# Kernel optimization log

Hardware: AMD Instinct MI355X
Metric: run time of the kernel (lower is better)

The kernel has to match this reference:

```python
import jax, jax.numpy as jnp
import numpy as np

# ---- static config (mirrors CE defaults) ----
PS = 7        # patch size
WS = 27       # search window (per side)
S0 = 4        # query stride (stride0)
KS = 100      # k_s: top-k kept by search
KA = 100      # k_a: top-k used for aggregation
SCALE = 10.0  # softmax_scale
CI = 16       # inter_channels


def conv2d(x, w, b, pad):
    y = jax.lax.conv_general_dilated(
        x, w, (1, 1), [(pad, pad), (pad, pad)],
        dimension_numbers=("NCHW", "OIHW", "NCHW"))
    return y + b[None, :, None, None]


def all_patches(v):
    """[T,C,H,W] -> [T, H*W, C*PS*PS]; top-left anchored PSxPS patches,
    edge-clamped at the border (dnls-style bounded patch extraction)."""
    t, c, h, w = v.shape
    ii = jnp.clip(jnp.arange(h)[:, None] + jnp.arange(PS)[None, :], 0, h - 1)
    jj = jnp.clip(jnp.arange(w)[:, None] + jnp.arange(PS)[None, :], 0, w - 1)
    p = v[:, :, ii][:, :, :, :, jj]          # [T,C,H,PS,W,PS]
    p = p.transpose(0, 2, 4, 1, 3, 5)        # [T,H,W,C,PS,PS]
    return p.reshape(t, h * w, c * PS * PS)


def setup_inputs():
    key = jax.random.key(0)
    ks = jax.random.split(key, 4)
    vid = jax.random.normal(ks[0], (4, 64, 128, 128), jnp.float32)
    g_w = jax.random.normal(ks[1], (CI, 64, 3, 3), jnp.float32) * 0.05
    g_b = jnp.zeros((CI,), jnp.float32)
    theta_w = jax.random.normal(ks[2], (CI, 64, 1, 1), jnp.float32) * 0.1
    theta_b = jnp.zeros((CI,), jnp.float32)
    return {"vid": vid, "g_w": g_w, "g_b": g_b,
            "theta_w": theta_w, "theta_b": theta_b}


def reference(vid, g_w, g_b, theta_w, theta_b):
    t, c, h, w = vid.shape
    nH, nW = h // S0, w // S0
    Q, N = nH * nW, h * w

    # feature extraction (g -> search features, theta -> aggregation values)
    v1 = conv2d(vid, g_w, g_b, 1)          # [T,CI,H,W]
    v2 = conv2d(vid, theta_w, theta_b, 0)  # [T,CI,H,W]

    # windowed k-NN patch search: query grid (stride0) vs all keys (stride1=1)
    P1 = all_patches(v1)                                    # [T,N,D]
    qis = jnp.arange(nH) * S0
    qjs = jnp.arange(nW) * S0
    qflat = (qis[:, None] * w + qjs[None, :]).reshape(-1)   # [Q]
    Pq = P1[:, qflat]                                       # [T,Q,D]
    scores = jnp.einsum("tqd,tnd->tqn", Pq, P1)             # [T,Q,N]

    off = jnp.arange(WS) - WS // 2
    ci = jnp.clip(qis[:, None] + off, 0, h - 1)             # [nH,WS]
    cj = jnp.clip(qjs[:, None] + off, 0, w - 1)             # [nW,WS]
    cand = (ci[:, None, :, None] * w + cj[None, :, None, :]).reshape(Q, WS * WS)
    dists = jnp.take_along_axis(scores, cand[None], axis=2)  # [T,Q,WS*WS]

    d_k, widx = jax.lax.top_k(dists, KS)                    # [T,Q,KS]
    inds = jnp.take_along_axis(jnp.broadcast_to(cand[None], dists.shape),
                               widx, axis=2)                # flat key positions

    # top-k softmax aggregation weights
    wgt = jax.nn.softmax(d_k[..., :KA] * SCALE, axis=-1)    # [T,Q,KA]
    inds_a = inds[..., :KA]

    # wpsum: weighted sum of value patches gathered at neighbor indices,
    # expressed as sparse-scatter matrix @ dense patch matrix
    A = jnp.zeros((t, Q, N), scores.dtype).at[
        jnp.arange(t)[:, None, None],
        jnp.arange(Q)[None, :, None],
        inds_a].add(wgt)                                    # [T,Q,N]
    P2 = all_patches(v2)                                    # [T,N,D]
    z = jnp.einsum("tqn,tnd->tqd", A, P2)                   # [T,Q,CI*PS*PS]

    # ifold: scatter-add overlapping patches + count normalization
    z = z.reshape(t, Q, CI, PS, PS).transpose(0, 2, 1, 3, 4)
    z = z.reshape(t, CI, Q * PS * PS)
    ri = jnp.clip(qis[:, None] + jnp.arange(PS), 0, h - 1)  # [nH,PS]
    rj = jnp.clip(qjs[:, None] + jnp.arange(PS), 0, w - 1)  # [nW,PS]
    pix = (ri[:, None, :, None] * w + rj[None, :, None, :]).reshape(-1)
    Y = jnp.zeros((t, CI, N), z.dtype).at[:, :, pix].add(z)
    Zc = jnp.zeros((N,), z.dtype).at[pix].add(1.0)
    y = (Y / Zc).reshape(t, CI, h, w)
    return y
```

## Files before the change

kernel.cpp:

```cpp
#include <hip/hip_runtime.h>
#include <hip/hip_bf16.h>

#define T_ 4
#define C_ 64
#define H_ 128
#define W_ 128
#define CI_ 16
#define PS_ 7
#define NC_ 729
#define NCP_ 732
#define S0_ 4
#define KS_ 100
#define NQ_ 1024
#define SCALE_ 10.0f
#define HW_ (H_*W_)
#define RW_ 45
#define LCAP_ 768
#define CB_ 8
#define CH_ 32

typedef float v2f __attribute__((ext_vector_type(2)));
#if __has_builtin(__builtin_elementwise_fma)
#define VFMA(a, b, c) __builtin_elementwise_fma((a), (b), (c))
#else
#define VFMA(a, b, c) ((a) * (b) + (c))
#endif

__device__ __forceinline__ float4 f4add(float4 a, float4 b) {
  return make_float4(a.x + b.x, a.y + b.y, a.z + b.z, a.w + b.w);
}

__device__ __forceinline__ float4 colfix(float4 r, bool loB, bool hiB) {
  float4 o;
  o.x = loB ? 0.f : (hiB ? r.y : r.x);
  o.y = loB ? r.x : (hiB ? r.z : r.y);
  o.z = loB ? r.y : (hiB ? r.w : r.z);
  o.w = loB ? r.z : (hiB ? 0.f : r.w);
  return o;
}

__global__ __launch_bounds__(128, 1) void conv_fused_kernel(
    const float* __restrict__ vid, const float* __restrict__ gw,
    const float* __restrict__ gb, const float* __restrict__ tw,
    const float* __restrict__ tb, float4* __restrict__ v1A,
    float4* __restrict__ v1B, float4* __restrict__ v2A,
    float4* __restrict__ v2B) {
  __shared__ float wls[CH_ * 9 * 4];
  __shared__ float tls[CH_ * 4];
  const int tid = threadIdx.x;
  const int g = blockIdx.y;
  const int t = blockIdx.z & 3, half = blockIdx.z >> 2;
  for (int m = tid; m < CH_ * 9 * 4; m += 128) {
    int co = m & 3, ck = m >> 2;
    wls[m] = gw[((size_t)(g * 4 + co) * C_) * 9 + half * (CH_ * 9) + ck];
  }
  for (int m = tid; m < CH_ * 4; m += 128) {
    int o = m & 3, c = m >> 2;
    tls[m] = tw[(g * 4 + o) * C_ + half * CH_ + c];
  }
  __syncthreads();
  const int ti0 = (blockIdx.x >> 3) * 16, tj0 = (blockIdx.x & 7) * 16;
  const int u = tid >> 3, v = tid & 7;
  const int i = ti0 + u, j0 = tj0 + 2 * v;
  const int c0 = j0 - 1;
  const int c0c = min(max(c0, 0), W_ - 4);
  const bool loB = (c0 < 0), hiB = (c0 > W_ - 4);
  const int rm1 = max(i - 1, 0), rp1 = min(i + 1, H_ - 1);
  const float mk0 = (i > 0) ? 1.f : 0.f;
  const float mk2 = (i < H_ - 1) ? 1.f : 0.f;
  const int o0 = rm1 * W_ + c0c, o1 = i * W_ + c0c, o2 = rp1 * W_ + c0c;

  float accA[4], accB[4], acc1A[4], acc1B[4];
#pragma unroll
  for (int co = 0; co < 4; ++co) {
    float bg = half ? 0.f : gb[g * 4 + co];
    float bt = half ? 0.f : tb[g * 4 + co];
    accA[co] = bg; accB[co] = bg;
    acc1A[co] = bt; acc1B[co] = bt;
  }

  const float* vb = vid + ((size_t)t * C_ + half * CH_) * HW_;
#pragma unroll 1
  for (int cb = 0; cb < CH_; cb += CB_) {
    float4 r[CB_][3];
#pragma unroll
    for (int c = 0; c < CB_; ++c) {
      const float* p = vb + (size_t)(cb + c) * HW_;
      r[c][0] = *(const float4*)(p + o0);
      r[c][1] = *(const float4*)(p + o1);
      r[c][2] = *(const float4*)(p + o2);
    }
#pragma unroll
    for (int c = 0; c < CB_; ++c) {
      float4 f0 = colfix(r[c][0], loB, hiB);
      float4 f1 = colfix(r[c][1], loB, hiB);
      float4 f2 = colfix(r[c][2], loB, hiB);
      f0.x *= mk0; f0.y *= mk0; f0.z *= mk0; f0.w *= mk0;
      f2.x *= mk2; f2.y *= mk2; f2.z *= mk2; f2.w *= mk2;
      const float* wc = &wls[(cb + c) * 36];
      const float* tc = &tls[(cb + c) * 4];
      float e0[4] = {f0.x, f0.y, f0.z, f0.w};
      float e1[4] = {f1.x, f1.y, f1.z, f1.w};
      float e2[4] = {f2.x, f2.y, f2.z, f2.w};
#pragma unroll
      for (int co = 0; co < 4; ++co) {
        acc1A[co] = fmaf(tc[co], e1[1], acc1A[co]);
        acc1B[co] = fmaf(tc[co], e1[2], acc1B[co]);
      }
#pragma unroll
      for (int kj = 0; kj < 3; ++kj) {
#pragma unroll
        for (int co = 0; co < 4; ++co) {
          accA[co] = fmaf(wc[(0 * 3 + kj) * 4 + co], e0[kj],     accA[co]);
          accB[co] = fmaf(wc[(0 * 3 + kj) * 4 + co], e0[kj + 1], accB[co]);
          accA[co] = fmaf(wc[(1 * 3 + kj) * 4 + co], e1[kj],     accA[co]);
          accB[co] = fmaf(wc[(1 * 3 + kj) * 4 + co], e1[kj + 1], accB[co]);
          accA[co] = fmaf(wc[(2 * 3 + kj) * 4 + co], e2[kj],     accA[co]);
          accB[co] = fmaf(wc[(2 * 3 + kj) * 4 + co], e2[kj + 1], accB[co]);
        }
      }
    }
  }
  float4* v1o = half ? v1B : v1A;
  float4* v2o = half ? v2B : v2A;
  const size_t o = ((size_t)g * T_ + t) * HW_ + i * W_ + j0;
  v1o[o]     = make_float4(accA[0], accA[1], accA[2], accA[3]);
  v1o[o + 1] = make_float4(accB[0], accB[1], accB[2], accB[3]);
  v2o[o]     = make_float4(acc1A[0], acc1A[1], acc1A[2], acc1A[3]);
  v2o[o + 1] = make_float4(acc1B[0], acc1B[1], acc1B[2], acc1B[3]);
}

__global__ __launch_bounds__(512, 2) void dist_kernel(
    const float4* __restrict__ v1A, const float4* __restrict__ v1B,
    float* __restrict__ out, int cbase, int nch) {
  __shared__ float4 Rs[2][2048];
  const int tid = threadIdx.x;
  const int t = blockIdx.y;
  const int qi0 = (blockIdx.x >> 3) * 16, qj0 = (blockIdx.x & 7) * 16;
  const int w = tid >> 6, lane = tid & 63;
  const int pr = w >> 2, dj = (w & 3) * 4;
  const int rbase = 8 * pr;
  const int qi_p = qi0 + rbase;
  const int qj = qj0 + dj;
  const int la = lane >> 1, bg = lane & 1;
  const int b_lo = max(13 - qj, 0);
  const int bs = bg ? 13 : b_lo;
  const int a_lo0 = max(13 - qi_p, 0);
  const int a_lo1 = max(9 - qi_p, 0);
  const bool compute_ok = (la < 31);

  int soff[4];
#pragma unroll
  for (int k = 0; k < 4; ++k) {
    int p = min(tid + 512 * k, RW_ * RW_ - 1);
    int uu = p / RW_, vv = p - uu * RW_;
    int row = min(max(qi0 - 13 + uu, 0), H_ - 1);
    int col = min(max(qj0 - 13 + vv, 0), W_ - 1);
    soff[k] = row * W_ + col;
  }

  v2f acc0[14], acc1[14];
#pragma unroll
  for (int j = 0; j < 14; ++j) { acc0[j] = (v2f){0.f, 0.f}; acc1[j] = (v2f){0.f, 0.f}; }

  float4 st[4];
  {
    const float4* sA = v1A + ((size_t)cbase * T_ + t) * HW_;
    const float4* sB = v1B + ((size_t)cbase * T_ + t) * HW_;
#pragma unroll
    for (int k = 0; k < 4; ++k) st[k] = f4add(sA[soff[k]], sB[soff[k]]);
  }
  int cur = 0;
#pragma unroll 1
  for (int ci = 0; ci < nch; ++ci) {
    float4* buf = &Rs[cur][0];
#pragma unroll
    for (int k = 0; k < 4; ++k) buf[tid + 512 * k] = st[k];
    if (ci + 1 < nch) {
      const float4* sA = v1A + ((size_t)(cbase + ci + 1) * T_ + t) * HW_;
      const float4* sB = v1B + ((size_t)(cbase + ci + 1) * T_ + t) * HW_;
#pragma unroll
      for (int k = 0; k < 4; ++k) st[k] = f4add(sA[soff[k]], sB[soff[k]]);
    }
    __syncthreads();
    if (compute_ok) {
#pragma unroll 1
      for (int r = 0; r < 7; ++r) {
        v2f q0lo[7], q0hi[7], q1lo[7], q1hi[7];
        const float4* q0row = &buf[(rbase + 13 + r) * RW_ + dj + 13];
#pragma unroll
        for (int s = 0; s < 7; ++s) {
          float4 qq = q0row[s];
          q0lo[s] = (v2f){qq.x, qq.y};
          q0hi[s] = (v2f){qq.z, qq.w};
          float4 q2 = q0row[4 * RW_ + s];
          q1lo[s] = (v2f){q2.x, q2.y};
          q1hi[s] = (v2f){q2.z, q2.w};
        }
        const float4* crow = &buf[(rbase + la + r) * RW_ + dj + bs];
#pragma unroll
        for (int y = 0; y < 20; ++y) {
          float4 vv4 = crow[y];
          v2f vlo = (v2f){vv4.x, vv4.y}, vhi = (v2f){vv4.z, vv4.w};
          const int s_lo = (y > 13) ? (y - 13) : 0;
          const int s_hi = (y < 6) ? y : 6;
#pragma unroll
          for (int s = s_lo; s <= s_hi; ++s) {
            int j = y - s;
            acc0[j] = VFMA(q0lo[s], vlo, acc0[j]);
            acc0[j] = VFMA(q0hi[s], vhi, acc0[j]);
            acc1[j] = VFMA(q1lo[s], vlo, acc1[j]);
            acc1[j] = VFMA(q1hi[s], vhi, acc1[j]);
          }
        }
      }
    }
    cur ^= 1;
  }
  if (compute_ok) {
    const int q0q = ((qi_p >> 2) << 5) + (qj >> 2);
    if (la >= a_lo0 && la <= 26) {
      float* o = out + ((size_t)t * NQ_ + q0q) * NCP_ + la * 27 + bs;
#pragma unroll
      for (int j = 0; j < 14; ++j) o[j] = acc0[j].x + acc0[j].y;
    }
    const int a1 = la - 4;
    if (a1 >= a_lo1 && a1 <= 26) {
      float* o = out + ((size_t)t * NQ_ + (q0q + 32)) * NCP_ + a1 * 27 + bs;
#pragma unroll
      for (int j = 0; j < 14; ++j) o[j] = acc1[j].x + acc1[j].y;
    }
  }
}

__global__ __launch_bounds__(256) void select_kernel(
    const float* __restrict__ distA, const float* __restrict__ distB, int dual,
    int* __restrict__ sel_n, float* __restrict__ sel_w,
    float* __restrict__ wsum_out) {
  __shared__ float dist[NC_];
  __shared__ unsigned int ukey[NC_];
  __shared__ float redf[4];
  __shared__ unsigned int hist[256];
  __shared__ int lk[LCAP_];
  __shared__ unsigned int lkey[LCAP_];
  __shared__ unsigned int scal[6];

  const int tid = threadIdx.x;
  const int lane = tid & 63, wid = tid >> 6;
  const int q = blockIdx.x, t = blockIdx.y;
  const int qi = (q >> 5) * S0_, qj = (q & 31) * S0_;
  const int a_lo = max(13 - qi, 0), b_lo = max(13 - qj, 0);
  const size_t base = ((size_t)t * NQ_ + q) * NCP_;

  for (int h = tid; h < 256; h += 256) hist[h] = 0;
  if (tid == 0) { scal[2] = 0; scal[3] = 0; }
  float lmax = -INFINITY;
  if (a_lo == 0 && b_lo == 0) {
    if (tid < 182) {
      float4 d4 = *(const float4*)(distA + base + 4 * tid);
      if (dual) {
        float4 b4 = *(const float4*)(distB + base + 4 * tid);
        d4.x += b4.x; d4.y += b4.y; d4.z += b4.z; d4.w += b4.w;
      }
      float dv[4] = {d4.x, d4.y, d4.z, d4.w};
#pragma unroll
      for (int e = 0; e < 4; ++e) {
        int k = 4 * tid + e;
        float d = dv[e];
        dist[k] = d;
        unsigned int u = __float_as_uint(d);
        ukey[k] = u ^ (((unsigned int)((int)u >> 31)) | 0x80000000u);
        lmax = fmaxf(lmax, d);
      }
    } else if (tid == 182) {
      float d = distA[base + 728];
      if (dual) d += distB[base + 728];
      dist[728] = d;
      unsigned int u = __float_as_uint(d);
      ukey[728] = u ^ (((unsigned int)((int)u >> 31)) | 0x80000000u);
      lmax = d;
    }
  } else {
    for (int k = tid; k < NC_; k += 256) {
      int aa = k / 27, bb = k - aa * 27;
      int kk = max(aa, a_lo) * 27 + max(bb, b_lo);
      float d = distA[base + kk];
      if (dual) d += distB[base + kk];
      dist[k] = d;
      unsigned int u = __float_as_uint(d);
      ukey[k] = u ^ (((unsigned int)((int)u >> 31)) | 0x80000000u);
      lmax = fmaxf(lmax, d);
    }
  }
#pragma unroll
  for (int off = 32; off > 0; off >>= 1)
    lmax = fmaxf(lmax, __shfl_down(lmax, off, 64));
  if (lane == 0) redf[wid] = lmax;
  __syncthreads();
  const float dmax = fmaxf(fmaxf(redf[0], redf[1]), fmaxf(redf[2], redf[3]));
  for (int k = tid; k < NC_; k += 256) atomicAdd(&hist[ukey[k] >> 24], 1u);
  __syncthreads();
  if (wid == 0) {
    int s4 = (int)(hist[lane * 4] + hist[lane * 4 + 1] + hist[lane * 4 + 2] + hist[lane * 4 + 3]);
    int s = s4;
#pragma unroll
    for (int off = 1; off < 64; off <<= 1) {
      int o = __shfl_down(s, off, 64);
      if (lane + off < 64) s += o;
    }
    int above = s - s4;
    if (above < KS_ && s >= KS_) {
      int run = above;
#pragma unroll
      for (int bb = 3; bb >= 0; --bb) {
        int h = (int)hist[lane * 4 + bb];
        if (run + h >= KS_) { scal[0] = (unsigned int)(lane * 4 + bb); scal[1] = (unsigned int)run; break; }
        run += h;
      }
    }
  }
  __syncthreads();
  const unsigned int beta = scal[0];
  const int run = (int)scal[1];
  for (int h = tid; h < 256; h += 256) hist[h] = 0;
  __syncthreads();
  for (int k = tid; k < NC_; k += 256)
    if ((ukey[k] >> 24) == beta) atomicAdd(&hist[(ukey[k] >> 16) & 0xFFu], 1u);
  __syncthreads();
  if (wid == 0) {
    int s4 = (int)(hist[lane * 4] + hist[lane * 4 + 1] + hist[lane * 4 + 2] + hist[lane * 4 + 3]);
    int s = s4;
#pragma unroll
    for (int off = 1; off < 64; off <<= 1) {
      int o = __shfl_down(s, off, 64);
      if (lane + off < 64) s += o;
    }
    int above = run + s - s4;
    if (above < KS_ && run + s >= KS_) {
      int r2 = above;
#pragma unroll
      for (int bb = 3; bb >= 0; --bb) {
        int h = (int)hist[lane * 4 + bb];
        if (r2 + h >= KS_) { scal[4] = (unsigned int)(lane * 4 + bb); scal[5] = (unsigned int)r2; break; }
        r2 += h;
      }
    }
  }
  __syncthreads();
  const unsigned int beta2 = scal[4];
  const int run2 = (int)scal[5];
  const size_t outb = ((size_t)t * NQ_ + q) * KS_;
  float lsum = 0.f;
  for (int k = tid; k < NC_; k += 256) {
    unsigned int key = ukey[k];
    unsigned int bin = key >> 24;
    bool sel = false, bdry = false;
    if (bin > beta) sel = true;
    else if (bin == beta) {
      unsigned int b2 = (key >> 16) & 0xFFu;
      if (b2 > beta2) sel = true;
      else if (b2 == beta2) bdry = true;
    }
    if (sel) {
      unsigned int slot = atomicAdd(&scal[2], 1u);
      int aa = k / 27, bb = k - aa * 27;
      int ni = min(max(qi + aa - 13, 0), H_ - 1);
      int nj = min(max(qj + bb - 13, 0), W_ - 1);
      float wv = __expf(SCALE_ * (dist[k] - dmax));
      sel_n[outb + slot] = (ni << 7) | nj;
      sel_w[outb + slot] = wv;
      lsum += wv;
    } else if (bdry) {
      unsigned int pos = atomicAdd(&scal[3], 1u);
      if (pos < LCAP_) { lk[pos] = k; lkey[pos] = key; }
    }
  }
  __syncthreads();
  const int L = min((int)scal[3], LCAP_);
  for (int i = tid; i < L; i += 256) {
    unsigned int key = lkey[i];
    int k = lk[i];
    int cnt = run2;
    for (int m = 0; m < L; ++m)
      cnt += (int)((lkey[m] > key) || (lkey[m] == key && lk[m] < k));
    if (cnt < KS_) {
      unsigned int slot = atomicAdd(&scal[2], 1u);
      int aa = k / 27, bb = k - aa * 27;
      int ni = min(max(qi + aa - 13, 0), H_ - 1);
      int nj = min(max(qj + bb - 13, 0), W_ - 1);
      float wv = __expf(SCALE_ * (dist[k] - dmax));
      sel_n[outb + slot] = (ni << 7) | nj;
      sel_w[outb + slot] = wv;
      lsum += wv;
    }
  }
#pragma unroll
  for (int off = 32; off > 0; off >>= 1) lsum += __shfl_down(lsum, off, 64);
  __syncthreads();
  if (lane == 0) redf[wid] = lsum;
  __syncthreads();
  if (tid == 0) wsum_out[t * NQ_ + q] = (redf[0] + redf[1]) + (redf[2] + redf[3]);
}

__device__ __forceinline__ int cov_axis(int x) {
  int c = 0;
#pragma unroll
  for (int r = 0; r < 7; ++r) {
    if (x < H_ - 1) {
      int qb = x - r;
      c += (qb >= 0 && (qb & 3) == 0) ? 1 : 0;
    } else {
      c += (r >= 3) ? 1 : 0;
    }
  }
  return c;
}

__global__ __launch_bounds__(1024) void agg_kernel(
    const float4* __restrict__ v2A, const float4* __restrict__ v2B,
    const int* __restrict__ sel_n, const float* __restrict__ sel_w,
    const float* __restrict__ wsum, float* __restrict__ Y) {
  __shared__ float4 Rs[RW_ * RW_];
  __shared__ int s_off[16][KS_];
  __shared__ float s_w[16][KS_];
  const int tid = threadIdx.x;
  const int t = blockIdx.y;
  const int qi0 = (blockIdx.x >> 3) * 16, qj0 = (blockIdx.x & 7) * 16;
  const int w = tid >> 6, lane = tid & 63;
  const int di = (w >> 2) * 4, dj = (w & 3) * 4;
  const int qi = qi0 + di, qj = qj0 + dj;
  const int q = ((qi >> 2) << 5) + (qj >> 2);
  const size_t base = ((size_t)t * NQ_ + q) * KS_;
  const float inv = 1.0f / wsum[t * NQ_ + q];
  for (int k = lane; k < KS_; k += 64) {
    int n = sel_n[base + k];
    int ni = n >> 7, nj = n & 127;
    s_off[w][k] = (ni - qi0 + 13) * RW_ + (nj - qj0 + 13);
    s_w[w][k] = sel_w[base + k] * inv;
  }
  const int r = lane / 7, s = lane - r * 7;
  const int myo = r * RW_ + s;
  const int oi = min(qi + r, H_ - 1), oj = min(qj + s, W_ - 1);
  const float invZ = 1.0f / (float)(cov_axis(oi) * cov_axis(oj));
#pragma unroll 1
  for (int cc = 0; cc < 4; ++cc) {
    __syncthreads();
    const float4* sA = v2A + ((size_t)cc * T_ + t) * HW_;
    const float4* sB = v2B + ((size_t)cc * T_ + t) * HW_;
    for (int p = tid; p < RW_ * RW_; p += 1024) {
      int uu = p / RW_, vv = p - uu * RW_;
      int row = min(max(qi0 - 13 + uu, 0), H_ - 1);
      int col = min(max(qj0 - 13 + vv, 0), W_ - 1);
      const int so = row * W_ + col;
      Rs[p] = f4add(sA[so], sB[so]);
    }
    __syncthreads();
    if (lane < 49) {
      float4 acc = make_float4(0.f, 0.f, 0.f, 0.f);
#pragma unroll 4
      for (int k = 0; k < KS_; ++k) {
        float wv = s_w[w][k];
        float4 v = Rs[s_off[w][k] + myo];
        acc.x = fmaf(wv, v.x, acc.x);
        acc.y = fmaf(wv, v.y, acc.y);
        acc.z = fmaf(wv, v.z, acc.z);
        acc.w = fmaf(wv, v.w, acc.w);
      }
      float* yb = Y + (((size_t)t * CI_ + cc * 4) * H_ + oi) * W_ + oj;
      atomicAdd(yb, acc.x * invZ);
      atomicAdd(yb + HW_, acc.y * invZ);
      atomicAdd(yb + 2 * HW_, acc.z * invZ);
      atomicAdd(yb + 3 * HW_, acc.w * invZ);
    }
  }
}

extern "C" void kernel_launch(void* const* d_in, const int* in_sizes, int n_in,
                              void* d_out, int out_size, void* d_ws, size_t ws_size,
                              hipStream_t stream) {
  const float* vid     = (const float*)d_in[0];
  const float* g_w     = (const float*)d_in[1];
  const float* g_b     = (const float*)d_in[2];
  const float* theta_w = (const float*)d_in[3];
  const float* theta_b = (const float*)d_in[4];
  float* Y = (float*)d_out;

  const size_t VSZ = (size_t)4 * T_ * HW_ * 4;
  float* v1A   = (float*)d_ws;
  float* v1B   = v1A + VSZ;
  float* v2A   = v1B + VSZ;
  float* v2B   = v2A + VSZ;
  float* distG = v2B + VSZ;
  int*   sel_n = (int*)(distG + (size_t)T_ * NQ_ * NCP_);
  float* sel_w = (float*)(sel_n + (size_t)T_ * NQ_ * KS_);
  float* wsumv = sel_w + (size_t)T_ * NQ_ * KS_;
  float* distB = wsumv + (size_t)T_ * NQ_;

  const size_t need_dual =
      (VSZ * 4 + (size_t)T_ * NQ_ * NCP_ * 2 +
       (size_t)T_ * NQ_ * KS_ * 2 + (size_t)T_ * NQ_) * sizeof(float);
  const int dual = (ws_size >= need_dual) ? 1 : 0;

  hipMemsetAsync(Y, 0, (size_t)out_size * sizeof(float), stream);

  conv_fused_kernel<<<dim3(64, 4, 2 * T_), 128, 0, stream>>>(
      vid, g_w, g_b, theta_w, theta_b,
      (float4*)v1A, (float4*)v1B, (float4*)v2A, (float4*)v2B);
  if (dual) {
    dist_kernel<<<dim3(64, T_), 512, 0, stream>>>(
        (const float4*)v1A, (const float4*)v1B, distG, 0, 2);
    dist_kernel<<<dim3(64, T_), 512, 0, stream>>>(
        (const float4*)v1A, (const float4*)v1B, distB, 2, 2);
  } else {
    dist_kernel<<<dim3(64, T_), 512, 0, stream>>>(
        (const float4*)v1A, (const float4*)v1B, distG, 0, 4);
  }
  select_kernel<<<dim3(NQ_, T_), 256, 0, stream>>>(distG, distB, dual, sel_n, sel_w, wsumv);
  agg_kernel<<<dim3(64, T_), 1024, 0, stream>>>(
      (const float4*)v2A, (const float4*)v2B, sel_n, sel_w, wsumv, Y);
}
```

Baseline: 256.4 us.

## Drop dual distance split and split aggregation across channel groups

Removes the workspace-dependent dual path, so one distance launch covers all four channel groups and the select kernel reads a single distance buffer instead of summing two. The aggregation kernel gains a grid z-dimension of 2, with each block handling two channel groups instead of four. This doubles the aggregation block count to fill more CUs. The cost is that each aggregation block reloads the selected indices and weights, and the distance kernel runs a longer serial channel loop in one launch.

```diff
diff --git a/kernel.cpp b/kernel.cpp
--- a/kernel.cpp
+++ b/kernel.cpp
@@ -132,7 +132,7 @@
 
 __global__ __launch_bounds__(512, 2) void dist_kernel(
     const float4* __restrict__ v1A, const float4* __restrict__ v1B,
-    float* __restrict__ out, int cbase, int nch) {
+    float* __restrict__ out) {
   __shared__ float4 Rs[2][2048];
   const int tid = threadIdx.x;
   const int t = blockIdx.y;
@@ -165,20 +165,20 @@
 
   float4 st[4];
   {
-    const float4* sA = v1A + ((size_t)cbase * T_ + t) * HW_;
-    const float4* sB = v1B + ((size_t)cbase * T_ + t) * HW_;
+    const float4* sA = v1A + ((size_t)0 * T_ + t) * HW_;
+    const float4* sB = v1B + ((size_t)0 * T_ + t) * HW_;
 #pragma unroll
     for (int k = 0; k < 4; ++k) st[k] = f4add(sA[soff[k]], sB[soff[k]]);
   }
   int cur = 0;
 #pragma unroll 1
-  for (int ci = 0; ci < nch; ++ci) {
+  for (int ci = 0; ci < 4; ++ci) {
     float4* buf = &Rs[cur][0];
 #pragma unroll
     for (int k = 0; k < 4; ++k) buf[tid + 512 * k] = st[k];
-    if (ci + 1 < nch) {
-      const float4* sA = v1A + ((size_t)(cbase + ci + 1) * T_ + t) * HW_;
-      const float4* sB = v1B + ((size_t)(cbase + ci + 1) * T_ + t) * HW_;
+    if (ci + 1 < 4) {
+      const float4* sA = v1A + ((size_t)(ci + 1) * T_ + t) * HW_;
+      const float4* sB = v1B + ((size_t)(ci + 1) * T_ + t) * HW_;
 #pragma unroll
       for (int k = 0; k < 4; ++k) st[k] = f4add(sA[soff[k]], sB[soff[k]]);
     }
@@ -234,9 +234,8 @@
 }
 
 __global__ __launch_bounds__(256) void select_kernel(
-    const float* __restrict__ distA, const float* __restrict__ distB, int dual,
-    int* __restrict__ sel_n, float* __restrict__ sel_w,
-    float* __restrict__ wsum_out) {
+    const float* __restrict__ distA, int* __restrict__ sel_n,
+    float* __restrict__ sel_w, float* __restrict__ wsum_out) {
   __shared__ float dist[NC_];
   __shared__ unsigned int ukey[NC_];
   __shared__ float redf[4];
@@ -258,10 +257,6 @@
   if (a_lo == 0 && b_lo == 0) {
     if (tid < 182) {
       float4 d4 = *(const float4*)(distA + base + 4 * tid);
-      if (dual) {
-        float4 b4 = *(const float4*)(distB + base + 4 * tid);
-        d4.x += b4.x; d4.y += b4.y; d4.z += b4.z; d4.w += b4.w;
-      }
       float dv[4] = {d4.x, d4.y, d4.z, d4.w};
 #pragma unroll
       for (int e = 0; e < 4; ++e) {
@@ -274,7 +269,6 @@
       }
     } else if (tid == 182) {
       float d = distA[base + 728];
-      if (dual) d += distB[base + 728];
       dist[728] = d;
       unsigned int u = __float_as_uint(d);
       ukey[728] = u ^ (((unsigned int)((int)u >> 31)) | 0x80000000u);
@@ -285,7 +279,6 @@
       int aa = k / 27, bb = k - aa * 27;
       int kk = max(aa, a_lo) * 27 + max(bb, b_lo);
       float d = distA[base + kk];
-      if (dual) d += distB[base + kk];
       dist[k] = d;
       unsigned int u = __float_as_uint(d);
       ukey[k] = u ^ (((unsigned int)((int)u >> 31)) | 0x80000000u);
@@ -425,6 +418,7 @@
   __shared__ float s_w[16][KS_];
   const int tid = threadIdx.x;
   const int t = blockIdx.y;
+  const int cc0 = blockIdx.z * 2;
   const int qi0 = (blockIdx.x >> 3) * 16, qj0 = (blockIdx.x & 7) * 16;
   const int w = tid >> 6, lane = tid & 63;
   const int di = (w >> 2) * 4, dj = (w & 3) * 4;
@@ -443,7 +437,8 @@
   const int oi = min(qi + r, H_ - 1), oj = min(qj + s, W_ - 1);
   const float invZ = 1.0f / (float)(cov_axis(oi) * cov_axis(oj));
 #pragma unroll 1
-  for (int cc = 0; cc < 4; ++cc) {
+  for (int ci = 0; ci < 2; ++ci) {
+    const int cc = cc0 + ci;
     __syncthreads();
     const float4* sA = v2A + ((size_t)cc * T_ + t) * HW_;
     const float4* sB = v2B + ((size_t)cc * T_ + t) * HW_;
@@ -494,28 +489,15 @@
   int*   sel_n = (int*)(distG + (size_t)T_ * NQ_ * NCP_);
   float* sel_w = (float*)(sel_n + (size_t)T_ * NQ_ * KS_);
   float* wsumv = sel_w + (size_t)T_ * NQ_ * KS_;
-  float* distB = wsumv + (size_t)T_ * NQ_;
-
-  const size_t need_dual =
-      (VSZ * 4 + (size_t)T_ * NQ_ * NCP_ * 2 +
-       (size_t)T_ * NQ_ * KS_ * 2 + (size_t)T_ * NQ_) * sizeof(float);
-  const int dual = (ws_size >= need_dual) ? 1 : 0;
 
   hipMemsetAsync(Y, 0, (size_t)out_size * sizeof(float), stream);
 
   conv_fused_kernel<<<dim3(64, 4, 2 * T_), 128, 0, stream>>>(
       vid, g_w, g_b, theta_w, theta_b,
       (float4*)v1A, (float4*)v1B, (float4*)v2A, (float4*)v2B);
-  if (dual) {
-    dist_kernel<<<dim3(64, T_), 512, 0, stream>>>(
-        (const float4*)v1A, (const float4*)v1B, distG, 0, 2);
-    dist_kernel<<<dim3(64, T_), 512, 0, stream>>>(
-        (const float4*)v1A, (const float4*)v1B, distB, 2, 2);
-  } else {
-    dist_kernel<<<dim3(64, T_), 512, 0, stream>>>(
-        (const float4*)v1A, (const float4*)v1B, distG, 0, 4);
-  }
-  select_kernel<<<dim3(NQ_, T_), 256, 0, stream>>>(distG, distB, dual, sel_n, sel_w, wsumv);
-  agg_kernel<<<dim3(64, T_), 1024, 0, stream>>>(
+  dist_kernel<<<dim3(64, T_), 512, 0, stream>>>(
+      (const float4*)v1A, (const float4*)v1B, distG);
+  select_kernel<<<dim3(NQ_, T_), 256, 0, stream>>>(distG, sel_n, sel_w, wsumv);
+  agg_kernel<<<dim3(64, T_, 2), 1024, 0, stream>>>(
       (const float4*)v2A, (const float4*)v2B, sel_n, sel_w, wsumv, Y);
 }
```

Measured after the change: 243.8 us, median of 3. -4.9%, faster.
